# Optimization experiments

Measured on AMD Instinct MI355X. Metric: run time of the kernel, lower is better.

The kernel has to match this reference:

```python
import jax, jax.numpy as jnp
import numpy as np

N = 500000
V = 50000
GF = 64
OC = 256

def _lin(key, din, dout):
    k1, k2 = jax.random.split(key)
    w = jax.random.normal(k1, (din, dout), dtype=jnp.float32) * 0.02
    b = jax.random.normal(k2, (dout,), dtype=jnp.float32) * 0.02
    return w, b

def setup_inputs() -> dict:
    key = jax.random.key(0)
    ks = jax.random.split(key, 12)
    inp_feat = jax.random.normal(ks[0], (N, 6), dtype=jnp.float32)
    vox2point_idx = jax.random.randint(ks[1], (N,), 0, V, dtype=jnp.int32)
    w1x, b1x = _lin(ks[2], 3, GF)
    w2x, b2x = _lin(ks[3], GF, OC // 8)
    w1r, b1r = _lin(ks[4], 3, GF)
    w2r, b2r = _lin(ks[5], GF, OC // 8)
    wax, bax = _lin(ks[6], OC // 4, OC // 8)
    war, bar = _lin(ks[7], OC // 4, OC // 8)
    wv1, bv1 = _lin(ks[8], OC // 2, OC // 2)
    w3, b3 = _lin(ks[9], OC, OC)
    w4, b4 = _lin(ks[10], OC, OC)
    wv2, bv2 = _lin(ks[11], OC, OC)
    return dict(inp_feat=inp_feat, vox2point_idx=vox2point_idx, num_vox=V,
                w1x=w1x, b1x=b1x, w2x=w2x, b2x=b2x,
                w1r=w1r, b1r=b1r, w2r=w2r, b2r=b2r,
                wax=wax, bax=bax, war=war, bar=bar,
                wv1=wv1, bv1=bv1, w3=w3, b3=b3, w4=w4, b4=b4,
                wv2=wv2, bv2=bv2)

def reference(inp_feat, vox2point_idx, num_vox,
              w1x, b1x, w2x, b2x, w1r, b1r, w2r, b2r,
              wax, bax, war, bar, wv1, bv1, w3, b3, w4, b4, wv2, bv2):
    relu = jax.nn.relu
    xyz = inp_feat[:, :3]
    rgb = inp_feat[:, 3:]
    fx = relu(relu(xyz @ w1x + b1x) @ w2x + b2x)   # [N, 32]
    fr = relu(relu(rgb @ w1r + b1r) @ w2r + b2r)   # [N, 32]
    comb = jnp.concatenate([fx, fr], axis=-1)       # [N, 64]
    pf2 = jnp.concatenate([
        fx, fx * jax.nn.sigmoid(comb @ wax + bax),
        fr, fr * jax.nn.sigmoid(comb @ war + bar)], axis=-1)  # [N, 128]
    # scatter-max to voxels; torch_scatter fills empty segments with 0 and
    # pf2 >= 0 elementwise, so clamp -inf (jax empty fill) to 0 for parity.
    vox = jax.ops.segment_max(pf2, vox2point_idx, num_segments=num_vox)
    vox = jnp.maximum(vox, 0.0)                     # [V, 128]
    vox = relu(vox @ wv1 + bv1)
    pg = vox[vox2point_idx]                          # gather back [N, 128]
    pf3 = jnp.concatenate([pg, pf2], axis=-1)        # [N, 256]
    pf5 = relu(relu(pf3 @ w3 + b3) @ w4 + b4)        # [N, 256]
    vox2 = jax.ops.segment_max(pf5, vox2point_idx, num_segments=num_vox)
    vox2 = jnp.maximum(vox2, 0.0)
    return relu(vox2 @ wv2 + bv2)                    # [V, 256]
```

## Files before the change

kernel.cpp:

```cpp
#include <hip/hip_runtime.h>

#define NPTS 500000
#define NVOX 50000
#define NBLK 196

typedef unsigned short u16;
typedef unsigned int u32;
typedef __attribute__((ext_vector_type(8))) short short8;
typedef __attribute__((ext_vector_type(4))) float floatx4;
typedef __attribute__((ext_vector_type(4))) unsigned int uintx4;
typedef __attribute__((ext_vector_type(2))) unsigned int uintx2;
typedef __attribute__((ext_vector_type(2))) unsigned short us2;

__device__ __forceinline__ u32 pkbf(float lo, float hi) {
    u32 r;
    asm("v_cvt_pk_bf16_f32 %0, %1, %2" : "=v"(r) : "v"(lo), "v"(hi));
    return r;
}
__device__ __forceinline__ u16 f2bf(float f) {
    u32 r;
    asm("v_cvt_pk_bf16_f32 %0, %1, %1" : "=v"(r) : "v"(f));
    return (u16)r;
}
__device__ __forceinline__ u32 pmax(u32 a, u32 b) {
    us2 r = __builtin_elementwise_max(__builtin_bit_cast(us2, a), __builtin_bit_cast(us2, b));
    return __builtin_bit_cast(u32, r);
}

__global__ void k_wtransform(const float* __restrict__ W, u16* __restrict__ Wf, int K, int N) {
    int t = blockIdx.x * 256 + threadIdx.x;
    if (t >= K * N) return;
    int k = t / N, n = t - k * N;
    int kk = k >> 5, q = (k >> 3) & 3, j = k & 7;
    Wf[((size_t)((kk * 4 + q) * N + n) << 3) + j] = f2bf(W[t]);
}

__global__ void k_wcat(const float* __restrict__ w2x, const float* __restrict__ w2r, u16* __restrict__ wcatf) {
    int t = blockIdx.x * 256 + threadIdx.x;
    if (t >= 128 * 64) return;
    int k = t >> 6, n = t & 63;
    float v;
    if (k < 64) v = (n < 32) ? w2x[k * 32 + n] : 0.f;
    else        v = (n >= 32) ? w2r[(k - 64) * 32 + (n - 32)] : 0.f;
    int kk = k >> 5, q = (k >> 3) & 3, j = k & 7;
    wcatf[((size_t)((kk * 4 + q) * 64 + n) << 3) + j] = f2bf(v);
}

__global__ void k_watt(const float* __restrict__ wax, const float* __restrict__ war, u16* __restrict__ wattf) {
    int t = blockIdx.x * 256 + threadIdx.x;
    if (t >= 64 * 64) return;
    int k = t >> 6, n = t & 63;
    float v = (n < 32) ? wax[k * 32 + n] : war[k * 32 + (n - 32)];
    int kk = k >> 5, q = (k >> 3) & 3, j = k & 7;
    wattf[((size_t)((kk * 4 + q) * 64 + n) << 3) + j] = f2bf(v);
}

__global__ void k_hist(const int* __restrict__ idx, int* __restrict__ hcnt) {
    int i = blockIdx.x * 256 + threadIdx.x;
    if (i < NPTS) atomicAdd(&hcnt[idx[i]], 1);
}

__global__ __launch_bounds__(256) void k_scan1(const int* __restrict__ hcnt, int* __restrict__ bsum) {
    __shared__ int wsum[4];
    int t = threadIdx.x;
    int i = blockIdx.x * 256 + t;
    int c = (i < NVOX) ? hcnt[i] : 0;
    #pragma unroll
    for (int d = 32; d >= 1; d >>= 1) c += __shfl_xor(c, d, 64);
    if ((t & 63) == 0) wsum[t >> 6] = c;
    __syncthreads();
    if (t == 0) bsum[blockIdx.x] = wsum[0] + wsum[1] + wsum[2] + wsum[3];
}

__global__ __launch_bounds__(256) void k_scan2(const int* __restrict__ bsum, int* __restrict__ boff) {
    __shared__ int wsum[4];
    int t = threadIdx.x, lane = t & 63, w = t >> 6;
    int c = (t < NBLK) ? bsum[t] : 0;
    int v = c;
    #pragma unroll
    for (int d = 1; d < 64; d <<= 1) {
        int o = __shfl_up(v, d, 64);
        if (lane >= d) v += o;
    }
    if (lane == 63) wsum[w] = v;
    __syncthreads();
    int wo = 0;
    #pragma unroll
    for (int k = 0; k < 4; k++) if (k < w) wo += wsum[k];
    if (t < NBLK) boff[t] = wo + v - c;
}

__global__ __launch_bounds__(256) void k_scan3(const int* __restrict__ hcnt, const int* __restrict__ boff,
                                               int* __restrict__ cur) {
    __shared__ int wsum[4];
    int t = threadIdx.x, lane = t & 63, w = t >> 6;
    int i = blockIdx.x * 256 + t;
    int c = (i < NVOX) ? hcnt[i] : 0;
    int v = c;
    #pragma unroll
    for (int d = 1; d < 64; d <<= 1) {
        int o = __shfl_up(v, d, 64);
        if (lane >= d) v += o;
    }
    if (lane == 63) wsum[w] = v;
    __syncthreads();
    int wo = 0;
    #pragma unroll
    for (int k = 0; k < 4; k++) if (k < w) wo += wsum[k];
    if (i < NVOX) cur[i] = boff[blockIdx.x] + wo + v - c;
}

__global__ void k_scatter(const int* __restrict__ idx, int* __restrict__ cur,
                          int* __restrict__ sptid, int* __restrict__ svid) {
    int i = blockIdx.x * 256 + threadIdx.x;
    if (i < NPTS) {
        int v = idx[i];
        int pos = atomicAdd(&cur[v], 1);
        sptid[pos] = i;
        svid[pos] = v;
    }
}

__global__ __launch_bounds__(512) void k_pointfeat(
    const float* __restrict__ inp, const int* __restrict__ sptid, const int* __restrict__ svid,
    const float* __restrict__ w1x, const float* __restrict__ b1x,
    const float* __restrict__ w1r, const float* __restrict__ b1r,
    const u16* __restrict__ wcatf, const float* __restrict__ b2x, const float* __restrict__ b2r,
    const u16* __restrict__ wattf, const float* __restrict__ bax, const float* __restrict__ bar,
    u16* __restrict__ pf2s, float* __restrict__ voxmax)
{
    __shared__ u16 hbuf[64 * 136];
    __shared__ u16 cbuf[64 * 72];
    __shared__ float wl[512];
    __shared__ int lvid[64];
    int t = threadIdx.x;
    int i0 = blockIdx.x * 64;
    int mcnt = NPTS - i0; if (mcnt > 64) mcnt = 64;
    {
        float v;
        if (t < 192)      v = w1x[t];
        else if (t < 256) v = b1x[t - 192];
        else if (t < 448) v = w1r[t - 256];
        else              v = b1r[t - 448];
        wl[t] = v;
    }
    if (t < 64) lvid[t] = (t < mcnt) ? svid[i0 + t] : -1;
    __syncthreads();
    {
        int m = t >> 3, c = t & 7;
        float x0 = 0, x1 = 0, x2 = 0, r0 = 0, r1 = 0, r2 = 0;
        if (m < mcnt) {
            const float* p = inp + (size_t)sptid[i0 + m] * 6;
            x0 = p[0]; x1 = p[1]; x2 = p[2]; r0 = p[3]; r1 = p[4]; r2 = p[5];
        }
        u16* hb = &hbuf[m * 136 + c * 8];
        #pragma unroll
        for (int jp = 0; jp < 4; jp++) {
            int c0 = c * 8 + 2 * jp, c1 = c0 + 1;
            float hx0 = fmaxf(wl[192 + c0] + x0 * wl[c0] + x1 * wl[64 + c0] + x2 * wl[128 + c0], 0.f);
            float hx1 = fmaxf(wl[192 + c1] + x0 * wl[c1] + x1 * wl[64 + c1] + x2 * wl[128 + c1], 0.f);
            float hr0 = fmaxf(wl[448 + c0] + r0 * wl[256 + c0] + r1 * wl[320 + c0] + r2 * wl[384 + c0], 0.f);
            float hr1 = fmaxf(wl[448 + c1] + r0 * wl[256 + c1] + r1 * wl[320 + c1] + r2 * wl[384 + c1], 0.f);
            *(u32*)(hb + 2 * jp)      = pkbf(hx0, hx1);
            *(u32*)(hb + 64 + 2 * jp) = pkbf(hr0, hr1);
        }
    }
    __syncthreads();
    int wave = t >> 6, l = t & 63, q = l >> 4, lm = l & 15;
    int g = wave & 3;
    int h2 = wave >> 2;
    int n = g * 16 + lm;
    floatx4 acc[2];
    #pragma unroll
    for (int a = 0; a < 2; a++) acc[a] = (floatx4){0.f, 0.f, 0.f, 0.f};
    #pragma unroll
    for (int kk = 0; kk < 4; kk++) {
        short8 bfrag = *(const short8*)&wcatf[(size_t)((kk * 4 + q) * 64 + n) << 3];
        #pragma unroll
        for (int ti = 0; ti < 2; ti++) {
            int tm = h2 * 2 + ti;
            short8 afrag = *(const short8*)&hbuf[(tm * 16 + lm) * 136 + kk * 32 + q * 8];
            acc[ti] = __builtin_amdgcn_mfma_f32_16x16x32_bf16(afrag, bfrag, acc[ti], 0, 0, 0);
        }
    }
    float bv = (n < 32) ? b2x[n] : b2r[n - 32];
    float comb_keep[2][4];
    #pragma unroll
    for (int ti = 0; ti < 2; ti++)
        #pragma unroll
        for (int r = 0; r < 4; r++) {
            int tm = h2 * 2 + ti;
            float v = fmaxf(acc[ti][r] + bv, 0.f);
            comb_keep[ti][r] = v;
            int m = tm * 16 + q * 4 + r;
            cbuf[m * 72 + n] = f2bf(v);
        }
    __syncthreads();
    floatx4 acc2[2];
    #pragma unroll
    for (int a = 0; a < 2; a++) acc2[a] = (floatx4){0.f, 0.f, 0.f, 0.f};
    #pragma unroll
    for (int kk = 0; kk < 2; kk++) {
        short8 bfrag = *(const short8*)&wattf[(size_t)((kk * 4 + q) * 64 + n) << 3];
        #pragma unroll
        for (int ti = 0; ti < 2; ti++) {
            int tm = h2 * 2 + ti;
            short8 afrag = *(const short8*)&cbuf[(tm * 16 + lm) * 72 + kk * 32 + q * 8];
            acc2[ti] = __builtin_amdgcn_mfma_f32_16x16x32_bf16(afrag, bfrag, acc2[ti], 0, 0, 0);
        }
    }
    float bv2 = (n < 32) ? bax[n] : bar[n - 32];
    int pp = (n < 32) ? n : 32 + n;
    #pragma unroll
    for (int ti = 0; ti < 2; ti++)
        #pragma unroll
        for (int r = 0; r < 4; r++) {
            int tm = h2 * 2 + ti;
            float att = acc2[ti][r] + bv2;
            float sg = 1.f / (1.f + __expf(-att));
            float plain = comb_keep[ti][r];
            float gated = plain * sg;
            int m = tm * 16 + q * 4 + r;
            hbuf[m * 136 + pp] = f2bf(plain);
            hbuf[m * 136 + pp + 32] = f2bf(gated);
        }
    __syncthreads();
    {
        int row = t >> 3, seg = t & 7;
        if (row < mcnt) {
            const u16* src = &hbuf[row * 136 + seg * 16];
            u16* dst = pf2s + (size_t)(i0 + row) * 128 + seg * 16;
            *(uintx4*)dst = *(const uintx4*)src;
        }
    }
    {
        int c2 = t & 63;
        int h = t >> 6;
        int r0 = h * 8;
        int r1 = r0 + 8; if (r1 > mcnt) r1 = mcnt;
        u32 mm = 0;
        int pvid = -1;
        for (int r = r0; r < r1; r++) {
            int vid = lvid[r];
            if (vid != pvid) {
                if (pvid >= 0) {
                    int* addr = (int*)(voxmax + (size_t)pvid * 128 + 2 * c2);
                    if (mm << 16) atomicMax(addr, (int)(mm << 16));
                    if (mm & 0xffff0000u) atomicMax(addr + 1, (int)(mm & 0xffff0000u));
                }
                pvid = vid; mm = 0;
            }
            u32 u = *(const u32*)&hbuf[r * 136 + 2 * c2];
            mm = pmax(mm, u);
        }
        if (pvid >= 0) {
            int* addr = (int*)(voxmax + (size_t)pvid * 128 + 2 * c2);
            if (mm << 16) atomicMax(addr, (int)(mm << 16));
            if (mm & 0xffff0000u) atomicMax(addr + 1, (int)(mm & 0xffff0000u));
        }
    }
}

template<int K, int N, bool ABF16, bool OUT_BF16>
__global__ __launch_bounds__(256) void k_gemm_relu(
    const void* __restrict__ Ap, const u16* __restrict__ Wf,
    const float* __restrict__ bias, void* __restrict__ outp, int M)
{
    constexpr int STRIDE = K + 8;
    constexpr int TN = N / 64;
    constexpr int KSTEPS = K / 32;
    constexpr int CW = K / 4;
    __shared__ u16 lds[64 * STRIDE];
    int i0 = blockIdx.x * 64;
    int mcnt = M - i0; if (mcnt > 64) mcnt = 64;
    int t = threadIdx.x;
    {
        int row = t >> 2, cseg = t & 3;
        u16* dst = &lds[row * STRIDE + cseg * CW];
        if (row < mcnt) {
            if (ABF16) {
                const u16* src = (const u16*)Ap + (size_t)(i0 + row) * K + cseg * CW;
                #pragma unroll
                for (int c = 0; c < CW / 8; c++)
                    *(uintx4*)(dst + c * 8) = *(const uintx4*)(src + c * 8);
            } else {
                const float* src = (const float*)Ap + (size_t)(i0 + row) * K + cseg * CW;
                #pragma unroll
                for (int c = 0; c < CW / 8; c++) {
                    float4 v0 = *(const float4*)(src + c * 8);
                    float4 v1 = *(const float4*)(src + c * 8 + 4);
                    uintx4 rr = (uintx4){ pkbf(v0.x, v0.y), pkbf(v0.z, v0.w),
                                          pkbf(v1.x, v1.y), pkbf(v1.z, v1.w) };
                    *(uintx4*)(dst + c * 8) = rr;
                }
            }
        } else {
            short8 z = {0, 0, 0, 0, 0, 0, 0, 0};
            #pragma unroll
            for (int c = 0; c < CW / 8; c++) *(short8*)(dst + c * 8) = z;
        }
    }
    __syncthreads();
    int wave = t >> 6, l = t & 63;
    int q = l >> 4, lm = l & 15;
    int wn0 = wave * (N / 4);
    floatx4 acc[4][TN];
    #pragma unroll
    for (int a = 0; a < 4; a++)
        #pragma unroll
        for (int b = 0; b < TN; b++) acc[a][b] = (floatx4){0.f, 0.f, 0.f, 0.f};
    #pragma unroll
    for (int kk = 0; kk < KSTEPS; kk++) {
        short8 afrag[4], bfrag[TN];
        #pragma unroll
        for (int tm = 0; tm < 4; tm++)
            afrag[tm] = *(const short8*)&lds[(tm * 16 + lm) * STRIDE + kk * 32 + q * 8];
        #pragma unroll
        for (int tn = 0; tn < TN; tn++)
            bfrag[tn] = *(const short8*)&Wf[(size_t)((kk * 4 + q) * N + wn0 + tn * 16 + lm) * 8];
        #pragma unroll
        for (int tm = 0; tm < 4; tm++)
            #pragma unroll
            for (int tn = 0; tn < TN; tn++)
                acc[tm][tn] = __builtin_amdgcn_mfma_f32_16x16x32_bf16(afrag[tm], bfrag[tn], acc[tm][tn], 0, 0, 0);
    }
    #pragma unroll
    for (int tm = 0; tm < 4; tm++)
        #pragma unroll
        for (int tn = 0; tn < TN; tn++) {
            int n = wn0 + tn * 16 + lm;
            float bv = bias[n];
            #pragma unroll
            for (int r = 0; r < 4; r++) {
                int m = tm * 16 + q * 4 + r;
                if (m < mcnt) {
                    float v = fmaxf(acc[tm][tn][r] + bv, 0.f);
                    if (OUT_BF16) ((u16*)outp)[(size_t)(i0 + m) * N + n] = f2bf(v);
                    else          ((float*)outp)[(size_t)(i0 + m) * N + n] = v;
                }
            }
        }
}

__global__ __launch_bounds__(512) void k_pointmlp(
    const u16* __restrict__ voxf, const u16* __restrict__ pf2s, const int* __restrict__ svid,
    const u16* __restrict__ w3f, const float* __restrict__ b3,
    const u16* __restrict__ w4f, const float* __restrict__ b4,
    float* __restrict__ vox2)
{
    constexpr int STRIDE = 264;
    __shared__ u16 lds[64 * STRIDE];
    __shared__ int lvid[64];
    __shared__ float bl[512];
    int i0 = blockIdx.x * 64;
    int mcnt = NPTS - i0; if (mcnt > 64) mcnt = 64;
    int t = threadIdx.x;
    if (t < 64) lvid[t] = (t < mcnt) ? svid[i0 + t] : -1;
    bl[t] = (t < 256) ? b3[t] : b4[t - 256];
    {
        int row = t >> 3, j = t & 7;
        int sv = (row < mcnt) ? svid[i0 + row] : 0;
        u16* dstb = &lds[row * STRIDE + j * 16];
        uintx4 a0 = (uintx4){0,0,0,0}, a1 = a0, b0 = a0, b1 = a0;
        if (row < mcnt) {
            const u16* s0 = voxf + (size_t)sv * 128 + j * 16;
            const u16* s1 = pf2s + (size_t)(i0 + row) * 128 + j * 16;
            a0 = *(const uintx4*)s0; a1 = *(const uintx4*)(s0 + 8);
            b0 = *(const uintx4*)s1; b1 = *(const uintx4*)(s1 + 8);
        }
        *(uintx4*)(dstb) = a0;
        *(uintx4*)(dstb + 8) = a1;
        *(uintx4*)(dstb + 128) = b0;
        *(uintx4*)(dstb + 136) = b1;
    }
    __syncthreads();
    int wave = t >> 6, l = t & 63;
    int q = l >> 4, lm = l & 15;
    int wm0 = wave * 32;
    floatx4 acc[2][4];
    #pragma unroll
    for (int a = 0; a < 2; a++)
        #pragma unroll
        for (int b = 0; b < 4; b++) acc[a][b] = (floatx4){0.f, 0.f, 0.f, 0.f};
    #pragma unroll
    for (int kk = 0; kk < 8; kk++) {
        short8 wfrag[2], bfrag[4];
        #pragma unroll
        for (int tm = 0; tm < 2; tm++)
            wfrag[tm] = *(const short8*)&w3f[(size_t)((kk * 4 + q) * 256 + wm0 + tm * 16 + lm) * 8];
        #pragma unroll
        for (int tn = 0; tn < 4; tn++)
            bfrag[tn] = *(const short8*)&lds[(tn * 16 + lm) * STRIDE + kk * 32 + q * 8];
        #pragma unroll
        for (int tm = 0; tm < 2; tm++)
            #pragma unroll
            for (int tn = 0; tn < 4; tn++)
                acc[tm][tn] = __builtin_amdgcn_mfma_f32_16x16x32_bf16(wfrag[tm], bfrag[tn], acc[tm][tn], 0, 0, 0);
    }
    __syncthreads();
    #pragma unroll
    for (int tm = 0; tm < 2; tm++) {
        float4 bq = *(const float4*)&bl[wm0 + tm * 16 + 4 * q];
        #pragma unroll
        for (int tn = 0; tn < 4; tn++) {
            u32 lo = pkbf(fmaxf(acc[tm][tn][0] + bq.x, 0.f), fmaxf(acc[tm][tn][1] + bq.y, 0.f));
            u32 hi = pkbf(fmaxf(acc[tm][tn][2] + bq.z, 0.f), fmaxf(acc[tm][tn][3] + bq.w, 0.f));
            *(uintx2*)&lds[(tn * 16 + lm) * STRIDE + wm0 + tm * 16 + 4 * q] = (uintx2){lo, hi};
        }
    }
    __syncthreads();
    floatx4 acc2[2][4];
    #pragma unroll
    for (int a = 0; a < 2; a++)
        #pragma unroll
        for (int b = 0; b < 4; b++) acc2[a][b] = (floatx4){0.f, 0.f, 0.f, 0.f};
    #pragma unroll
    for (int kk = 0; kk < 8; kk++) {
        short8 wfrag[2], bfrag[4];
        #pragma unroll
        for (int tm = 0; tm < 2; tm++)
            wfrag[tm] = *(const short8*)&w4f[(size_t)((kk * 4 + q) * 256 + wm0 + tm * 16 + lm) * 8];
        #pragma unroll
        for (int tn = 0; tn < 4; tn++)
            bfrag[tn] = *(const short8*)&lds[(tn * 16 + lm) * STRIDE + kk * 32 + q * 8];
        #pragma unroll
        for (int tm = 0; tm < 2; tm++)
            #pragma unroll
            for (int tn = 0; tn < 4; tn++)
                acc2[tm][tn] = __builtin_amdgcn_mfma_f32_16x16x32_bf16(wfrag[tm], bfrag[tn], acc2[tm][tn], 0, 0, 0);
    }
    __syncthreads();
    #pragma unroll
    for (int tm = 0; tm < 2; tm++) {
        float4 bq = *(const float4*)&bl[256 + wm0 + tm * 16 + 4 * q];
        #pragma unroll
        for (int tn = 0; tn < 4; tn++) {
            u32 lo = pkbf(fmaxf(acc2[tm][tn][0] + bq.x, 0.f), fmaxf(acc2[tm][tn][1] + bq.y, 0.f));
            u32 hi = pkbf(fmaxf(acc2[tm][tn][2] + bq.z, 0.f), fmaxf(acc2[tm][tn][3] + bq.w, 0.f));
            *(uintx2*)&lds[(tn * 16 + lm) * STRIDE + wm0 + tm * 16 + 4 * q] = (uintx2){lo, hi};
        }
    }
    __syncthreads();
    {
        int c2 = t & 127;
        int h = t >> 7;
        int r0 = h * 16;
        int r1 = r0 + 16; if (r1 > mcnt) r1 = mcnt;
        u32 mm = 0;
        int pvid = -1;
        for (int r = r0; r < r1; r++) {
            int vid = lvid[r];
            if (vid != pvid) {
                if (pvid >= 0) {
                    int* addr = (int*)(vox2 + (size_t)pvid * 256 + 2 * c2);
                    if (mm << 16) atomicMax(addr, (int)(mm << 16));
                    if (mm & 0xffff0000u) atomicMax(addr + 1, (int)(mm & 0xffff0000u));
                }
                pvid = vid; mm = 0;
            }
            u32 u = *(const u32*)&lds[r * STRIDE + 2 * c2];
            mm = pmax(mm, u);
        }
        if (pvid >= 0) {
            int* addr = (int*)(vox2 + (size_t)pvid * 256 + 2 * c2);
            if (mm << 16) atomicMax(addr, (int)(mm << 16));
            if (mm & 0xffff0000u) atomicMax(addr + 1, (int)(mm & 0xffff0000u));
        }
    }
}

extern "C" void kernel_launch(void* const* d_in, const int* in_sizes, int n_in,
                              void* d_out, int out_size, void* d_ws, size_t ws_size,
                              hipStream_t stream) {
    const float* inp = (const float*)d_in[0];
    const int*   idx = (const int*)d_in[1];
    const float* w1x = (const float*)d_in[3];  const float* b1x = (const float*)d_in[4];
    const float* w2x = (const float*)d_in[5];  const float* b2x = (const float*)d_in[6];
    const float* w1r = (const float*)d_in[7];  const float* b1r = (const float*)d_in[8];
    const float* w2r = (const float*)d_in[9];  const float* b2r = (const float*)d_in[10];
    const float* wax = (const float*)d_in[11]; const float* bax = (const float*)d_in[12];
    const float* war = (const float*)d_in[13]; const float* bar = (const float*)d_in[14];
    const float* wv1 = (const float*)d_in[15]; const float* bv1 = (const float*)d_in[16];
    const float* w3  = (const float*)d_in[17]; const float* b3  = (const float*)d_in[18];
    const float* w4  = (const float*)d_in[19]; const float* b4  = (const float*)d_in[20];
    const float* wv2 = (const float*)d_in[21]; const float* bv2 = (const float*)d_in[22];
    float* out = (float*)d_out;

    char* ws = (char*)d_ws;
    u16*   pf2s   = (u16*)ws;   ws += (size_t)NPTS * 128 * sizeof(u16);
    float* voxmax = (float*)ws; ws += (size_t)NVOX * 128 * sizeof(float);
    u16*   voxf   = (u16*)ws;   ws += (size_t)NVOX * 128 * sizeof(u16);
    float* vox2   = (float*)ws; ws += (size_t)NVOX * 256 * sizeof(float);
    u16*   w3f    = (u16*)ws;   ws += 65536 * sizeof(u16);
    u16*   w4f    = (u16*)ws;   ws += 65536 * sizeof(u16);
    u16*   wv1f   = (u16*)ws;   ws += 16384 * sizeof(u16);
    u16*   wv2f   = (u16*)ws;   ws += 65536 * sizeof(u16);
    u16*   wcatf  = (u16*)ws;   ws += 8192 * sizeof(u16);
    u16*   wattf  = (u16*)ws;   ws += 4096 * sizeof(u16);
    int*   hcnt   = (int*)ws;   ws += (size_t)NVOX * sizeof(int);
    int*   cur    = (int*)ws;   ws += (size_t)NVOX * sizeof(int);
    int*   bsum   = (int*)ws;   ws += (size_t)NBLK * sizeof(int);
    int*   boff   = (int*)ws;   ws += (size_t)NBLK * sizeof(int);
    int*   sptid  = (int*)ws;   ws += (size_t)NPTS * sizeof(int);
    int*   svid   = (int*)ws;   ws += (size_t)NPTS * sizeof(int);

    hipMemsetAsync(hcnt, 0, (size_t)NVOX * sizeof(int), stream);
    hipMemsetAsync(voxmax, 0, (size_t)NVOX * 128 * sizeof(float), stream);
    hipMemsetAsync(vox2, 0, (size_t)NVOX * 256 * sizeof(float), stream);

    k_wtransform<<<256, 256, 0, stream>>>(w3, w3f, 256, 256);
    k_wtransform<<<256, 256, 0, stream>>>(w4, w4f, 256, 256);
    k_wtransform<<<64,  256, 0, stream>>>(wv1, wv1f, 128, 128);
    k_wtransform<<<256, 256, 0, stream>>>(wv2, wv2f, 256, 256);
    k_wcat<<<32, 256, 0, stream>>>(w2x, w2r, wcatf);
    k_watt<<<16, 256, 0, stream>>>(wax, war, wattf);

    k_hist<<<(NPTS + 255) / 256, 256, 0, stream>>>(idx, hcnt);
    k_scan1<<<NBLK, 256, 0, stream>>>(hcnt, bsum);
    k_scan2<<<1, 256, 0, stream>>>(bsum, boff);
    k_scan3<<<NBLK, 256, 0, stream>>>(hcnt, boff, cur);
    k_scatter<<<(NPTS + 255) / 256, 256, 0, stream>>>(idx, cur, sptid, svid);

    k_pointfeat<<<(NPTS + 63) / 64, 512, 0, stream>>>(
        inp, sptid, svid, w1x, b1x, w1r, b1r, wcatf, b2x, b2r, wattf, bax, bar, pf2s, voxmax);

    k_gemm_relu<128, 128, false, true><<<(NVOX + 63) / 64, 256, 0, stream>>>(
        (const void*)voxmax, wv1f, bv1, (void*)voxf, NVOX);

    k_pointmlp<<<(NPTS + 63) / 64, 512, 0, stream>>>(
        voxf, pf2s, svid, w3f, b3, w4f, b4, vox2);

    k_gemm_relu<256, 256, false, false><<<(NVOX + 63) / 64, 256, 0, stream>>>(
        (const void*)vox2, wv2f, bv2, (void*)out, NVOX);
}
```

Measured before the change: 483.9 us.

## Fuse weight-prep launches, pre-sort input features in scatter, halve atomicMax threads

Merges the six weight-transform kernels and the hcnt memset into one launch, which cuts launch and host overhead. The scatter kernel now writes the input features themselves into sorted order, so point-feature loads are coalesced and no longer go through an indirect sptid lookup. The voxel max-reduction uses 256 threads with 16-row runs, so fewer atomics are issued because longer runs of equal voxel ids merge. The trade-off is an extra 12 MB buffer and scattered writes in k_scatter.

Result: slower. 500.8 us (+3.5%).

```diff
diff --git a/kernel.cpp b/kernel.cpp
--- a/kernel.cpp
+++ b/kernel.cpp
@@ -27,32 +27,50 @@
     return __builtin_bit_cast(u32, r);
 }
 
-__global__ void k_wtransform(const float* __restrict__ W, u16* __restrict__ Wf, int K, int N) {
-    int t = blockIdx.x * 256 + threadIdx.x;
-    if (t >= K * N) return;
+__device__ __forceinline__ void wt_one(const float* __restrict__ W, u16* __restrict__ Wf,
+                                       int N, int t, int KN) {
+    if (t >= KN) return;
     int k = t / N, n = t - k * N;
     int kk = k >> 5, q = (k >> 3) & 3, j = k & 7;
     Wf[((size_t)((kk * 4 + q) * N + n) << 3) + j] = f2bf(W[t]);
 }
 
-__global__ void k_wcat(const float* __restrict__ w2x, const float* __restrict__ w2r, u16* __restrict__ wcatf) {
-    int t = blockIdx.x * 256 + threadIdx.x;
-    if (t >= 128 * 64) return;
-    int k = t >> 6, n = t & 63;
-    float v;
-    if (k < 64) v = (n < 32) ? w2x[k * 32 + n] : 0.f;
-    else        v = (n >= 32) ? w2r[(k - 64) * 32 + (n - 32)] : 0.f;
-    int kk = k >> 5, q = (k >> 3) & 3, j = k & 7;
-    wcatf[((size_t)((kk * 4 + q) * 64 + n) << 3) + j] = f2bf(v);
-}
-
-__global__ void k_watt(const float* __restrict__ wax, const float* __restrict__ war, u16* __restrict__ wattf) {
-    int t = blockIdx.x * 256 + threadIdx.x;
-    if (t >= 64 * 64) return;
-    int k = t >> 6, n = t & 63;
-    float v = (n < 32) ? wax[k * 32 + n] : war[k * 32 + (n - 32)];
-    int kk = k >> 5, q = (k >> 3) & 3, j = k & 7;
-    wattf[((size_t)((kk * 4 + q) * 64 + n) << 3) + j] = f2bf(v);
+__global__ __launch_bounds__(256) void k_prep(
+    const float* __restrict__ w3, u16* __restrict__ w3f,
+    const float* __restrict__ w4, u16* __restrict__ w4f,
+    const float* __restrict__ wv1, u16* __restrict__ wv1f,
+    const float* __restrict__ wv2, u16* __restrict__ wv2f,
+    const float* __restrict__ w2x, const float* __restrict__ w2r, u16* __restrict__ wcatf,
+    const float* __restrict__ wax, const float* __restrict__ war, u16* __restrict__ wattf,
+    int* __restrict__ hcnt)
+{
+    int b = blockIdx.x, tid = threadIdx.x;
+    if (b < 256) {
+        wt_one(w3, w3f, 256, b * 256 + tid, 65536);
+    } else if (b < 512) {
+        wt_one(w4, w4f, 256, (b - 256) * 256 + tid, 65536);
+    } else if (b < 576) {
+        wt_one(wv1, wv1f, 128, (b - 512) * 256 + tid, 16384);
+    } else if (b < 832) {
+        wt_one(wv2, wv2f, 256, (b - 576) * 256 + tid, 65536);
+    } else if (b < 864) {
+        int t = (b - 832) * 256 + tid;
+        int k = t >> 6, n = t & 63;
+        float v;
+        if (k < 64) v = (n < 32) ? w2x[k * 32 + n] : 0.f;
+        else        v = (n >= 32) ? w2r[(k - 64) * 32 + (n - 32)] : 0.f;
+        int kk = k >> 5, q = (k >> 3) & 3, j = k & 7;
+        wcatf[((size_t)((kk * 4 + q) * 64 + n) << 3) + j] = f2bf(v);
+    } else if (b < 880) {
+        int t = (b - 864) * 256 + tid;
+        int k = t >> 6, n = t & 63;
+        float v = (n < 32) ? wax[k * 32 + n] : war[k * 32 + (n - 32)];
+        int kk = k >> 5, q = (k >> 3) & 3, j = k & 7;
+        wattf[((size_t)((kk * 4 + q) * 64 + n) << 3) + j] = f2bf(v);
+    } else {
+        int i = (b - 880) * 256 + tid;
+        if (i < NVOX) hcnt[i] = 0;
+    }
 }
 
 __global__ void k_hist(const int* __restrict__ idx, int* __restrict__ hcnt) {
@@ -111,18 +129,22 @@
 }
 
 __global__ void k_scatter(const int* __restrict__ idx, int* __restrict__ cur,
-                          int* __restrict__ sptid, int* __restrict__ svid) {
+                          const float* __restrict__ inp,
+                          float* __restrict__ inps, int* __restrict__ svid) {
     int i = blockIdx.x * 256 + threadIdx.x;
     if (i < NPTS) {
         int v = idx[i];
         int pos = atomicAdd(&cur[v], 1);
-        sptid[pos] = i;
         svid[pos] = v;
+        const float2* s = (const float2*)(inp + (size_t)i * 6);
+        float2 a = s[0], b = s[1], c = s[2];
+        float2* d = (float2*)(inps + (size_t)pos * 6);
+        d[0] = a; d[1] = b; d[2] = c;
     }
 }
 
 __global__ __launch_bounds__(512) void k_pointfeat(
-    const float* __restrict__ inp, const int* __restrict__ sptid, const int* __restrict__ svid,
+    const float* __restrict__ inps, const int* __restrict__ svid,
     const float* __restrict__ w1x, const float* __restrict__ b1x,
     const float* __restrict__ w1r, const float* __restrict__ b1r,
     const u16* __restrict__ wcatf, const float* __restrict__ b2x, const float* __restrict__ b2r,
@@ -150,7 +172,7 @@
         int m = t >> 3, c = t & 7;
         float x0 = 0, x1 = 0, x2 = 0, r0 = 0, r1 = 0, r2 = 0;
         if (m < mcnt) {
-            const float* p = inp + (size_t)sptid[i0 + m] * 6;
+            const float* p = inps + (size_t)(i0 + m) * 6;
             x0 = p[0]; x1 = p[1]; x2 = p[2]; r0 = p[3]; r1 = p[4]; r2 = p[5];
         }
         u16* hb = &hbuf[m * 136 + c * 8];
@@ -233,11 +255,11 @@
             *(uintx4*)dst = *(const uintx4*)src;
         }
     }
-    {
+    if (t < 256) {
         int c2 = t & 63;
         int h = t >> 6;
-        int r0 = h * 8;
-        int r1 = r0 + 8; if (r1 > mcnt) r1 = mcnt;
+        int r0 = h * 16;
+        int r1 = r0 + 16; if (r1 > mcnt) r1 = mcnt;
         u32 mm = 0;
         int pvid = -1;
         for (int r = r0; r < r1; r++) {
@@ -491,6 +513,7 @@
     float* voxmax = (float*)ws; ws += (size_t)NVOX * 128 * sizeof(float);
     u16*   voxf   = (u16*)ws;   ws += (size_t)NVOX * 128 * sizeof(u16);
     float* vox2   = (float*)ws; ws += (size_t)NVOX * 256 * sizeof(float);
+    float* inps   = (float*)ws; ws += (size_t)NPTS * 6 * sizeof(float);
     u16*   w3f    = (u16*)ws;   ws += 65536 * sizeof(u16);
     u16*   w4f    = (u16*)ws;   ws += 65536 * sizeof(u16);
     u16*   wv1f   = (u16*)ws;   ws += 16384 * sizeof(u16);
@@ -501,28 +524,22 @@
     int*   cur    = (int*)ws;   ws += (size_t)NVOX * sizeof(int);
     int*   bsum   = (int*)ws;   ws += (size_t)NBLK * sizeof(int);
     int*   boff   = (int*)ws;   ws += (size_t)NBLK * sizeof(int);
-    int*   sptid  = (int*)ws;   ws += (size_t)NPTS * sizeof(int);
     int*   svid   = (int*)ws;   ws += (size_t)NPTS * sizeof(int);
 
-    hipMemsetAsync(hcnt, 0, (size_t)NVOX * sizeof(int), stream);
     hipMemsetAsync(voxmax, 0, (size_t)NVOX * 128 * sizeof(float), stream);
     hipMemsetAsync(vox2, 0, (size_t)NVOX * 256 * sizeof(float), stream);
 
-    k_wtransform<<<256, 256, 0, stream>>>(w3, w3f, 256, 256);
-    k_wtransform<<<256, 256, 0, stream>>>(w4, w4f, 256, 256);
-    k_wtransform<<<64,  256, 0, stream>>>(wv1, wv1f, 128, 128);
-    k_wtransform<<<256, 256, 0, stream>>>(wv2, wv2f, 256, 256);
-    k_wcat<<<32, 256, 0, stream>>>(w2x, w2r, wcatf);
-    k_watt<<<16, 256, 0, stream>>>(wax, war, wattf);
+    k_prep<<<1076, 256, 0, stream>>>(w3, w3f, w4, w4f, wv1, wv1f, wv2, wv2f,
+                                     w2x, w2r, wcatf, wax, war, wattf, hcnt);
 
     k_hist<<<(NPTS + 255) / 256, 256, 0, stream>>>(idx, hcnt);
     k_scan1<<<NBLK, 256, 0, stream>>>(hcnt, bsum);
     k_scan2<<<1, 256, 0, stream>>>(bsum, boff);
     k_scan3<<<NBLK, 256, 0, stream>>>(hcnt, boff, cur);
-    k_scatter<<<(NPTS + 255) / 256, 256, 0, stream>>>(idx, cur, sptid, svid);
+    k_scatter<<<(NPTS + 255) / 256, 256, 0, stream>>>(idx, cur, inp, inps, svid);
 
     k_pointfeat<<<(NPTS + 63) / 64, 512, 0, stream>>>(
-        inp, sptid, svid, w1x, b1x, w1r, b1r, wcatf, b2x, b2r, wattf, bax, bar, pf2s, voxmax);
+        inps, svid, w1x, b1x, w1r, b1r, wcatf, b2x, b2r, wattf, bax, bar, pf2s, voxmax);
 
     k_gemm_relu<128, 128, false, true><<<(NVOX + 63) / 64, 256, 0, stream>>>(
         (const void*)voxmax, wv1f, bv1, (void*)voxf, NVOX);
```
